# Optimization experiments

Measured on AMD Instinct MI355X. Metric: run time of the kernel, lower is better.

The kernel has to match this reference:

```python
import jax, jax.numpy as jnp
import numpy as np

COSINE_SIM_SCALE = 8.0  # default scale in flash-cosine-sim-attention
LN_EPS = 1e-5
HEADS = 8

def _l2norm(t, eps=1e-12):
    return t * jax.lax.rsqrt(jnp.sum(t * t, axis=-1, keepdims=True) + eps)

def setup_inputs() -> dict:
    key = jax.random.key(0)
    k1, k2, k3 = jax.random.split(key, 3)
    b, n, dim = 2, 2048, 1024
    inner = 512  # heads * dim_head
    return {
        "x": jax.random.normal(k1, (b, n, dim), dtype=jnp.float32),
        "ln_w": jnp.ones((dim,), dtype=jnp.float32),
        "ln_b": jnp.zeros((dim,), dtype=jnp.float32),
        "w_qkv": jax.random.normal(k2, (dim, 3 * inner), dtype=jnp.float32) * 0.02,
        "w_out": jax.random.normal(k3, (inner, dim), dtype=jnp.float32) * 0.02,
    }

def reference(x, ln_w, ln_b, w_qkv, w_out):
    b, n, dim = x.shape
    h = HEADS
    # LayerNorm
    mu = jnp.mean(x, axis=-1, keepdims=True)
    var = jnp.mean(jnp.square(x - mu), axis=-1, keepdims=True)
    xn = (x - mu) * jax.lax.rsqrt(var + LN_EPS) * ln_w + ln_b
    # QKV projection, split into heads: b n (h d) -> b h n d
    qkv = xn @ w_qkv
    q, k, v = jnp.split(qkv, 3, axis=-1)
    def to_heads(t):
        return t.reshape(b, n, h, -1).transpose(0, 2, 1, 3)
    q, k, v = map(to_heads, (q, k, v))
    # cosine-sim attention: l2-normalize q, k then scaled dot product
    q = _l2norm(q)
    k = _l2norm(k)
    sim = jnp.einsum('bhid,bhjd->bhij', q, k) * COSINE_SIM_SCALE
    causal_mask = jnp.tril(jnp.ones((n, n), dtype=bool))
    sim = jnp.where(causal_mask, sim, jnp.finfo(sim.dtype).min)
    attn = jax.nn.softmax(sim, axis=-1)
    o = jnp.einsum('bhij,bhjd->bhid', attn, v)
    # b h n d -> b n (h d)
    o = o.transpose(0, 2, 1, 3).reshape(b, n, -1)
    return o @ w_out
```

## Files before the change

### kernel.cpp

```cpp
#include <hip/hip_runtime.h>
#include <hip/hip_bf16.h>

typedef __attribute__((ext_vector_type(8))) __bf16 bf16x8;
typedef __attribute__((ext_vector_type(4))) __bf16 bf16x4;
typedef __attribute__((ext_vector_type(4))) float f32x4;

#define B_     2
#define N_     2048
#define DIM_   1024
#define INNER_ 512
#define H_     8
#define DH_    64
#define ROWS_  (B_ * N_)
#define QKVN_  (3 * INNER_)
#define SEGROWS_ 5120

static __device__ __forceinline__ f32x4 mfma16(bf16x8 a, bf16x8 b, f32x4 c) {
    return __builtin_amdgcn_mfma_f32_16x16x32_bf16(a, b, c, 0, 0, 0);
}

static __device__ __forceinline__ void gld_lds16(const void* g, void* l) {
    __builtin_amdgcn_global_load_lds((const __attribute__((address_space(1))) void*)g,
                                     (__attribute__((address_space(3))) void*)l, 16, 0, 0);
}

__global__ __launch_bounds__(256) void ln_kernel(const float* __restrict__ x,
                                                 const float* __restrict__ w,
                                                 const float* __restrict__ bb,
                                                 __bf16* __restrict__ xn) {
    int row = blockIdx.x;
    int tid = threadIdx.x;
    const float* xr = x + (size_t)row * DIM_;
    f32x4 xv = *reinterpret_cast<const f32x4*>(xr + tid * 4);
    float s  = xv.x + xv.y + xv.z + xv.w;
    float sq = xv.x * xv.x + xv.y * xv.y + xv.z * xv.z + xv.w * xv.w;
#pragma unroll
    for (int m = 1; m < 64; m <<= 1) {
        s  += __shfl_xor(s, m);
        sq += __shfl_xor(sq, m);
    }
    __shared__ float red[2][4];
    int wid = tid >> 6, lane = tid & 63;
    if (lane == 0) { red[0][wid] = s; red[1][wid] = sq; }
    __syncthreads();
    s  = red[0][0] + red[0][1] + red[0][2] + red[0][3];
    sq = red[1][0] + red[1][1] + red[1][2] + red[1][3];
    float mu   = s * (1.0f / DIM_);
    float var  = sq * (1.0f / DIM_) - mu * mu;
    float rstd = rsqrtf(var + 1e-5f);
    f32x4 wv = *reinterpret_cast<const f32x4*>(w  + tid * 4);
    f32x4 bv = *reinterpret_cast<const f32x4*>(bb + tid * 4);
    bf16x4 o;
#pragma unroll
    for (int j = 0; j < 4; ++j) o[j] = (__bf16)((xv[j] - mu) * rstd * wv[j] + bv[j]);
    *reinterpret_cast<bf16x4*>(xn + (size_t)row * DIM_ + tid * 4) = o;
}

__global__ __launch_bounds__(256) void transpose_cast(const float* __restrict__ in,
                                                      __bf16* __restrict__ out,
                                                      int K, int N) {
    __shared__ float t[64][65];
    int n0 = blockIdx.x * 64, k0 = blockIdx.y * 64;
    int w = threadIdx.x >> 6, lane = threadIdx.x & 63;
#pragma unroll
    for (int i = 0; i < 16; ++i) {
        int k = 16 * w + i;
        t[k][lane] = in[(size_t)(k0 + k) * N + n0 + lane];
    }
    __syncthreads();
#pragma unroll
    for (int i = 0; i < 16; ++i) {
        int n = 16 * w + i;
        out[(size_t)(n0 + n) * K + k0 + lane] = (__bf16)t[lane][n];
    }
}

__global__ __launch_bounds__(256) void gemm_qkv(const __bf16* __restrict__ A,
                                                const __bf16* __restrict__ Bt,
                                                __bf16* __restrict__ Qh,
                                                __bf16* __restrict__ Kh,
                                                __bf16* __restrict__ Vrow) {
    const int K = DIM_;
    __shared__ __bf16 As[128 * 32];
    __shared__ __bf16 Bs[128 * 32];
    int tid = threadIdx.x;
    int w = tid >> 6, lane = tid & 63;
    int lr = lane & 15, lg = lane >> 4;
    int m0 = blockIdx.y * 128, n0 = blockIdx.x * 128;
    int wm = (w >> 1) * 64, wn = (w & 1) * 64;
    int srow = tid >> 2, sc = tid & 3;
    const __bf16* Ab = A  + (size_t)m0 * K;
    const __bf16* Bb = Bt + (size_t)n0 * K;
    f32x4 acc[4][4];
#pragma unroll
    for (int mi = 0; mi < 4; ++mi)
#pragma unroll
        for (int ci = 0; ci < 4; ++ci) acc[mi][ci] = f32x4{0.f, 0.f, 0.f, 0.f};
    for (int k0 = 0; k0 < K; k0 += 32) {
        __syncthreads();
#pragma unroll
        for (int q = 0; q < 2; ++q) {
            int row = q * 64 + srow;
            int cs = sc ^ (row & 3);
            gld_lds16(Ab + (size_t)row * K + k0 + 8 * cs, &As[(size_t)row * 32 + sc * 8]);
            gld_lds16(Bb + (size_t)row * K + k0 + 8 * cs, &Bs[(size_t)row * 32 + sc * 8]);
        }
        __syncthreads();
        bf16x8 af[4], bfr[4];
#pragma unroll
        for (int mi = 0; mi < 4; ++mi) {
            int r = wm + 16 * mi + lr;
            af[mi] = *reinterpret_cast<const bf16x8*>(&As[r * 32 + 8 * (lg ^ (r & 3))]);
        }
#pragma unroll
        for (int ci = 0; ci < 4; ++ci) {
            int r = wn + 16 * ci + lr;
            bfr[ci] = *reinterpret_cast<const bf16x8*>(&Bs[r * 32 + 8 * (lg ^ (r & 3))]);
        }
#pragma unroll
        for (int mi = 0; mi < 4; ++mi)
#pragma unroll
            for (int ci = 0; ci < 4; ++ci)
                acc[mi][ci] = mfma16(af[mi], bfr[ci], acc[mi][ci]);
    }
    int u = (n0 + wn) >> 6;
    bool isV = (u >= 16);
    float smul = (u < 8) ? 8.0f : 1.0f;
    __bf16* base;
    if (u < 8)       base = Qh   + (size_t)u * N_ * DH_;
    else if (u < 16) base = Kh   + (size_t)(u - 8) * N_ * DH_;
    else             base = Vrow + (size_t)(u - 16) * N_ * DH_;
#pragma unroll
    for (int mi = 0; mi < 4; ++mi)
#pragma unroll
        for (int r = 0; r < 4; ++r) {
            int grow = m0 + wm + 16 * mi + 4 * lg + r;
            int b = grow >> 11, n = grow & 2047;
            float sc2 = 1.0f;
            if (!isV) {
                float t = 0.f;
#pragma unroll
                for (int ci = 0; ci < 4; ++ci) t += acc[mi][ci][r] * acc[mi][ci][r];
#pragma unroll
                for (int m = 1; m < 16; m <<= 1) t += __shfl_xor(t, m);
                sc2 = rsqrtf(t + 1e-12f) * smul;
            }
            __bf16* dst = base + ((size_t)b * H_ * N_ + n) * DH_;
#pragma unroll
            for (int ci = 0; ci < 4; ++ci)
                dst[16 * ci + lr] = (__bf16)(acc[mi][ci][r] * sc2);
        }
}

template <typename OutT>
__global__ __launch_bounds__(256) void gemm_bt(const __bf16* __restrict__ A,
                                               const __bf16* __restrict__ Bt,
                                               OutT* __restrict__ C,
                                               int M, int N, int K) {
    __shared__ __bf16 As[128 * 32];
    __shared__ __bf16 Bs[128 * 32];
    int tid = threadIdx.x;
    int w = tid >> 6, lane = tid & 63;
    int lr = lane & 15, lg = lane >> 4;
    int m0 = blockIdx.y * 128, n0 = blockIdx.x * 128;
    int wm = (w >> 1) * 64, wn = (w & 1) * 64;
    int srow = tid >> 2, sc = tid & 3;
    const __bf16* Ab = A  + (size_t)m0 * K;
    const __bf16* Bb = Bt + (size_t)n0 * K;
    f32x4 acc[4][4];
#pragma unroll
    for (int mi = 0; mi < 4; ++mi)
#pragma unroll
        for (int ci = 0; ci < 4; ++ci) acc[mi][ci] = f32x4{0.f, 0.f, 0.f, 0.f};
    for (int k0 = 0; k0 < K; k0 += 32) {
        __syncthreads();
#pragma unroll
        for (int q = 0; q < 2; ++q) {
            int row = q * 64 + srow;
            int cs = sc ^ (row & 3);
            gld_lds16(Ab + (size_t)row * K + k0 + 8 * cs, &As[(size_t)row * 32 + sc * 8]);
            gld_lds16(Bb + (size_t)row * K + k0 + 8 * cs, &Bs[(size_t)row * 32 + sc * 8]);
        }
        __syncthreads();
        bf16x8 af[4], bfr[4];
#pragma unroll
        for (int mi = 0; mi < 4; ++mi) {
            int r = wm + 16 * mi + lr;
            af[mi] = *reinterpret_cast<const bf16x8*>(&As[r * 32 + 8 * (lg ^ (r & 3))]);
        }
#pragma unroll
        for (int ci = 0; ci < 4; ++ci) {
            int r = wn + 16 * ci + lr;
            bfr[ci] = *reinterpret_cast<const bf16x8*>(&Bs[r * 32 + 8 * (lg ^ (r & 3))]);
        }
#pragma unroll
        for (int mi = 0; mi < 4; ++mi)
#pragma unroll
            for (int ci = 0; ci < 4; ++ci)
                acc[mi][ci] = mfma16(af[mi], bfr[ci], acc[mi][ci]);
    }
#pragma unroll
    for (int mi = 0; mi < 4; ++mi)
#pragma unroll
        for (int ci = 0; ci < 4; ++ci)
#pragma unroll
            for (int r = 0; r < 4; ++r)
                C[(size_t)(m0 + wm + 16 * mi + 4 * lg + r) * N + n0 + wn + 16 * ci + lr] =
                    (OutT)acc[mi][ci][r];
}

__global__ __launch_bounds__(256) void vtrans(const __bf16* __restrict__ Vrow,
                                              __bf16* __restrict__ Vt) {
    __shared__ __bf16 t[64][66];
    int bh = blockIdx.y, n0 = blockIdx.x * 64;
    int w = threadIdx.x >> 6, lane = threadIdx.x & 63;
#pragma unroll
    for (int i = 0; i < 16; ++i) {
        int nl = 16 * w + i;
        t[nl][lane] = Vrow[((size_t)bh * N_ + n0 + nl) * DH_ + lane];
    }
    __syncthreads();
#pragma unroll
    for (int i = 0; i < 16; ++i) {
        int d = 16 * w + i;
        Vt[(size_t)bh * DH_ * N_ + (size_t)d * N_ + n0 + lane] = t[lane][d];
    }
}

__global__ __launch_bounds__(256) void attn_kernel(const __bf16* __restrict__ Qh,
                                                   const __bf16* __restrict__ Kh,
                                                   const __bf16* __restrict__ Vt,
                                                   float* __restrict__ Opart,
                                                   float* __restrict__ ml) {
    __shared__ __bf16 Ks[2][64 * 64];
    __shared__ __bf16 Vs[2][64 * 64];
    __shared__ __bf16 pl[4][16 * 64];
    int bh = blockIdx.x;
    int idx = blockIdx.y;
    int s, qt;
    if (idx < 32)      { s = 0; qt = 31 - idx; }
    else if (idx < 56) { s = 1; qt = 31 - (idx - 32); }
    else if (idx < 72) { s = 2; qt = 31 - (idx - 56); }
    else               { s = 3; qt = 31 - (idx - 72); }
    int jt0 = 8 * s;
    int jt1 = min(8 * s + 7, qt);
    int tid = threadIdx.x;
    int w = tid >> 6, lane = tid & 63;
    int lr = lane & 15, lg = lane >> 4;
    int qb = qt * 64;
    int qrow = qb + 16 * w;
    const __bf16* Qp = Qh + (size_t)bh * N_ * DH_;
    const __bf16* Kp = Kh + (size_t)bh * N_ * DH_;
    const __bf16* Vp = Vt + (size_t)bh * DH_ * N_;
    bf16x8 qf0 = *reinterpret_cast<const bf16x8*>(Qp + (size_t)(qrow + lr) * DH_ + 8 * lg);
    bf16x8 qf1 = *reinterpret_cast<const bf16x8*>(Qp + (size_t)(qrow + lr) * DH_ + 32 + 8 * lg);
    f32x4 oacc[4];
#pragma unroll
    for (int c = 0; c < 4; ++c) oacc[c] = f32x4{0.f, 0.f, 0.f, 0.f};
    float m_r[4], l_r[4];
#pragma unroll
    for (int r = 0; r < 4; ++r) { m_r[r] = -1e30f; l_r[r] = 0.f; }
    int srow = tid >> 3, sc = tid & 7;

    auto stage = [&](int buf, int jb) {
#pragma unroll
        for (int q = 0; q < 2; ++q) {
            int row = q * 32 + srow;
            int cs = sc ^ (row & 7);
            gld_lds16(Kp + (size_t)(jb + row) * DH_ + 8 * cs,
                      &Ks[buf][(size_t)row * 64 + sc * 8]);
            gld_lds16(Vp + (size_t)row * N_ + jb + 8 * cs,
                      &Vs[buf][(size_t)row * 64 + sc * 8]);
        }
    };

    stage(0, jt0 * 64);
    __syncthreads();
    int cur = 0;
    for (int jt = jt0; jt <= jt1; ++jt) {
        int jb = jt * 64;
        if (jt < jt1) stage(cur ^ 1, jb + 64);
        const __bf16* ks = &Ks[cur][0];
        const __bf16* vs = &Vs[cur][0];
        f32x4 sm[4];
#pragma unroll
        for (int ch = 0; ch < 4; ++ch) {
            int row = 16 * ch + lr;
            bf16x8 k0 = *reinterpret_cast<const bf16x8*>(&ks[row * 64 + 8 * (lg ^ (row & 7))]);
            bf16x8 k1 = *reinterpret_cast<const bf16x8*>(&ks[row * 64 + 8 * ((4 + lg) ^ (row & 7))]);
            f32x4 t = f32x4{0.f, 0.f, 0.f, 0.f};
            t = mfma16(qf0, k0, t);
            t = mfma16(qf1, k1, t);
            sm[ch] = t;
        }
        if (jt == qt) {
#pragma unroll
            for (int ch = 0; ch < 4; ++ch)
#pragma unroll
                for (int r = 0; r < 4; ++r) {
                    int qi = qrow + 4 * lg + r;
                    int j  = jb + 16 * ch + lr;
                    if (j > qi) sm[ch][r] = -1e30f;
                }
        }
        float fs[4];
#pragma unroll
        for (int r = 0; r < 4; ++r) {
            float pm = fmaxf(fmaxf(sm[0][r], sm[1][r]), fmaxf(sm[2][r], sm[3][r]));
#pragma unroll
            for (int msk = 1; msk < 16; msk <<= 1) pm = fmaxf(pm, __shfl_xor(pm, msk));
            float mn = fmaxf(m_r[r], pm);
            fs[r] = __expf(m_r[r] - mn);
            m_r[r] = mn;
        }
        f32x4 p[4];
#pragma unroll
        for (int ch = 0; ch < 4; ++ch)
#pragma unroll
            for (int r = 0; r < 4; ++r) p[ch][r] = __expf(sm[ch][r] - m_r[r]);
#pragma unroll
        for (int r = 0; r < 4; ++r) {
            float rs = p[0][r] + p[1][r] + p[2][r] + p[3][r];
#pragma unroll
            for (int msk = 1; msk < 16; msk <<= 1) rs += __shfl_xor(rs, msk);
            l_r[r] = l_r[r] * fs[r] + rs;
        }
#pragma unroll
        for (int dc = 0; dc < 4; ++dc)
#pragma unroll
            for (int r = 0; r < 4; ++r) oacc[dc][r] *= fs[r];
        __bf16* plw = &pl[w][0];
#pragma unroll
        for (int ch = 0; ch < 4; ++ch)
#pragma unroll
            for (int r = 0; r < 4; ++r) {
                int row = 4 * lg + r, col = 16 * ch + lr;
                plw[row * 64 + (((col >> 3) ^ (row & 7)) << 3) + (col & 7)] = (__bf16)p[ch][r];
            }
        bf16x8 pf0 = *reinterpret_cast<const bf16x8*>(&plw[lr * 64 + ((lg ^ (lr & 7)) << 3)]);
        bf16x8 pf1 = *reinterpret_cast<const bf16x8*>(&plw[lr * 64 + (((4 + lg) ^ (lr & 7)) << 3)]);
#pragma unroll
        for (int dc = 0; dc < 4; ++dc) {
            int row = 16 * dc + lr;
            bf16x8 v0 = *reinterpret_cast<const bf16x8*>(&vs[row * 64 + 8 * (lg ^ (row & 7))]);
            bf16x8 v1 = *reinterpret_cast<const bf16x8*>(&vs[row * 64 + 8 * ((4 + lg) ^ (row & 7))]);
            oacc[dc] = mfma16(pf0, v0, oacc[dc]);
            oacc[dc] = mfma16(pf1, v1, oacc[dc]);
        }
        __syncthreads();
        cur ^= 1;
    }
    int soff = 2048 * s - 256 * s * (s - 1);
#pragma unroll
    for (int r = 0; r < 4; ++r) {
        int n = qrow + 4 * lg + r;
        size_t ridx = (size_t)bh * SEGROWS_ + soff + (n - 512 * s);
#pragma unroll
        for (int dc = 0; dc < 4; ++dc)
            Opart[ridx * 64 + 16 * dc + lr] = oacc[dc][r];
        if (lr == 0) {
            ml[ridx * 2]     = m_r[r];
            ml[ridx * 2 + 1] = l_r[r];
        }
    }
}

__global__ __launch_bounds__(256) void combine_kernel(const float* __restrict__ Opart,
                                                      const float* __restrict__ ml,
                                                      __bf16* __restrict__ Obp) {
    int gid = blockIdx.x * 4 + (threadIdx.x >> 6);
    int lane = threadIdx.x & 63;
    int bh = gid >> 11, n = gid & 2047;
    int smax = n >> 9;
    float mstar = -1e30f;
#pragma unroll
    for (int s = 0; s < 4; ++s)
        if (s <= smax) {
            int soff = 2048 * s - 256 * s * (s - 1);
            size_t ridx = (size_t)bh * SEGROWS_ + soff + (n - 512 * s);
            mstar = fmaxf(mstar, ml[ridx * 2]);
        }
    float acc = 0.f, lsum = 0.f;
#pragma unroll
    for (int s = 0; s < 4; ++s)
        if (s <= smax) {
            int soff = 2048 * s - 256 * s * (s - 1);
            size_t ridx = (size_t)bh * SEGROWS_ + soff + (n - 512 * s);
            float wgt = __expf(ml[ridx * 2] - mstar);
            acc  += wgt * Opart[ridx * 64 + lane];
            lsum += wgt * ml[ridx * 2 + 1];
        }
    int b = bh >> 3, h = bh & 7;
    Obp[((size_t)(b * N_ + n)) * INNER_ + h * DH_ + lane] = (__bf16)(acc / lsum);
}

extern "C" void kernel_launch(void* const* d_in, const int* in_sizes, int n_in,
                              void* d_out, int out_size, void* d_ws, size_t ws_size,
                              hipStream_t stream) {
    const float* x    = (const float*)d_in[0];
    const float* lnw  = (const float*)d_in[1];
    const float* lnb  = (const float*)d_in[2];
    const float* wqkv = (const float*)d_in[3];
    const float* wout = (const float*)d_in[4];
    float* out = (float*)d_out;

    char* ws = (char*)d_ws;
    size_t off = 0;
    auto alloc = [&](size_t bytes) -> char* {
        char* p = ws + off;
        off += (bytes + 255) & ~(size_t)255;
        return p;
    };
    __bf16* xn    = (__bf16*)alloc((size_t)ROWS_ * DIM_ * 2);
    __bf16* wqkvT = (__bf16*)alloc((size_t)QKVN_ * DIM_ * 2);
    __bf16* woutT = (__bf16*)alloc((size_t)DIM_ * INNER_ * 2);
    __bf16* Qhp   = (__bf16*)alloc((size_t)B_ * H_ * N_ * DH_ * 2);
    __bf16* Khp   = (__bf16*)alloc((size_t)B_ * H_ * N_ * DH_ * 2);
    __bf16* Vrow  = (__bf16*)alloc((size_t)B_ * H_ * N_ * DH_ * 2);
    __bf16* Vtp   = (__bf16*)alloc((size_t)B_ * H_ * DH_ * N_ * 2);
    __bf16* Obp   = (__bf16*)alloc((size_t)ROWS_ * INNER_ * 2);
    float*  Opart = (float*)alloc((size_t)B_ * H_ * SEGROWS_ * DH_ * 4);
    float*  mlb   = (float*)alloc((size_t)B_ * H_ * SEGROWS_ * 2 * 4);
    if (off > ws_size) return;

    transpose_cast<<<dim3(QKVN_ / 64, DIM_ / 64), 256, 0, stream>>>(wqkv, wqkvT, DIM_, QKVN_);
    transpose_cast<<<dim3(DIM_ / 64, INNER_ / 64), 256, 0, stream>>>(wout, woutT, INNER_, DIM_);
    ln_kernel<<<ROWS_, 256, 0, stream>>>(x, lnw, lnb, xn);
    gemm_qkv<<<dim3(QKVN_ / 128, ROWS_ / 128), 256, 0, stream>>>(xn, wqkvT, Qhp, Khp, Vrow);
    vtrans<<<dim3(N_ / 64, B_ * H_), 256, 0, stream>>>(Vrow, Vtp);
    attn_kernel<<<dim3(B_ * H_, 80), 256, 0, stream>>>(Qhp, Khp, Vtp, Opart, mlb);
    combine_kernel<<<(ROWS_ * H_) / 4, 256, 0, stream>>>(Opart, mlb, Obp);
    gemm_bt<float><<<dim3(DIM_ / 128, ROWS_ / 128), 256, 0, stream>>>(Obp, woutT, out, ROWS_, DIM_, INNER_);
}
```

Baseline: 182.9 us.

## Use fixed softmax max from cosine-sim bound and compute row sums via MFMA

Because q and k are l2-normalized, scores are bounded by the scale, so the online-softmax running max is replaced by a fixed constant. Q is prescaled by 8*log2(e) so exp2 can be used directly. Row sums come from an extra MFMA against a ones vector instead of shuffle reductions. This removes the max/sum shuffles and rescaling in the attention kernel and the max pass in the combine kernel, and the grid is flattened to 1D. In exchange it relies on the cosine bound and risks underflow for rows whose scores sit far below the maximum.

```diff
diff --git a/kernel.cpp b/kernel.cpp
--- a/kernel.cpp
+++ b/kernel.cpp
@@ -14,6 +14,8 @@
 #define ROWS_  (B_ * N_)
 #define QKVN_  (3 * INNER_)
 #define SEGROWS_ 5120
+#define QSCALE_ 11.5415603f
+#define MAXL2_  11.5415603f
 
 static __device__ __forceinline__ f32x4 mfma16(bf16x8 a, bf16x8 b, f32x4 c) {
     return __builtin_amdgcn_mfma_f32_16x16x32_bf16(a, b, c, 0, 0, 0);
@@ -125,7 +127,7 @@
     }
     int u = (n0 + wn) >> 6;
     bool isV = (u >= 16);
-    float smul = (u < 8) ? 8.0f : 1.0f;
+    float smul = (u < 8) ? QSCALE_ : 1.0f;
     __bf16* base;
     if (u < 8)       base = Qh   + (size_t)u * N_ * DH_;
     else if (u < 16) base = Kh   + (size_t)(u - 8) * N_ * DH_;
@@ -231,35 +233,35 @@
                                                    const __bf16* __restrict__ Kh,
                                                    const __bf16* __restrict__ Vt,
                                                    float* __restrict__ Opart,
-                                                   float* __restrict__ ml) {
+                                                   float* __restrict__ lpart) {
     __shared__ __bf16 Ks[2][64 * 64];
     __shared__ __bf16 Vs[2][64 * 64];
     __shared__ __bf16 pl[4][16 * 64];
-    int bh = blockIdx.x;
-    int idx = blockIdx.y;
+    int bh  = blockIdx.x & 15;
+    int sid = blockIdx.x >> 4;
     int s, qt;
-    if (idx < 32)      { s = 0; qt = 31 - idx; }
-    else if (idx < 56) { s = 1; qt = 31 - (idx - 32); }
-    else if (idx < 72) { s = 2; qt = 31 - (idx - 56); }
-    else               { s = 3; qt = 31 - (idx - 72); }
+    if (sid < 32)      { s = 0; qt = 31 - sid; }
+    else if (sid < 56) { s = 1; qt = 31 - (sid - 32); }
+    else if (sid < 72) { s = 2; qt = 31 - (sid - 56); }
+    else               { s = 3; qt = 31 - (sid - 72); }
     int jt0 = 8 * s;
     int jt1 = min(8 * s + 7, qt);
     int tid = threadIdx.x;
     int w = tid >> 6, lane = tid & 63;
     int lr = lane & 15, lg = lane >> 4;
-    int qb = qt * 64;
-    int qrow = qb + 16 * w;
+    int qrow = qt * 64 + 16 * w;
     const __bf16* Qp = Qh + (size_t)bh * N_ * DH_;
     const __bf16* Kp = Kh + (size_t)bh * N_ * DH_;
     const __bf16* Vp = Vt + (size_t)bh * DH_ * N_;
     bf16x8 qf0 = *reinterpret_cast<const bf16x8*>(Qp + (size_t)(qrow + lr) * DH_ + 8 * lg);
     bf16x8 qf1 = *reinterpret_cast<const bf16x8*>(Qp + (size_t)(qrow + lr) * DH_ + 32 + 8 * lg);
+    bf16x8 ones;
+#pragma unroll
+    for (int j = 0; j < 8; ++j) ones[j] = (__bf16)1.0f;
     f32x4 oacc[4];
+    f32x4 oacc4 = f32x4{0.f, 0.f, 0.f, 0.f};
 #pragma unroll
     for (int c = 0; c < 4; ++c) oacc[c] = f32x4{0.f, 0.f, 0.f, 0.f};
-    float m_r[4], l_r[4];
-#pragma unroll
-    for (int r = 0; r < 4; ++r) { m_r[r] = -1e30f; l_r[r] = 0.f; }
     int srow = tid >> 3, sc = tid & 7;
 
     auto stage = [&](int buf, int jb) {
@@ -293,42 +295,20 @@
             t = mfma16(qf1, k1, t);
             sm[ch] = t;
         }
-        if (jt == qt) {
-#pragma unroll
-            for (int ch = 0; ch < 4; ++ch)
-#pragma unroll
-                for (int r = 0; r < 4; ++r) {
+        f32x4 p[4];
+        bool diag = (jt == qt);
+#pragma unroll
+        for (int ch = 0; ch < 4; ++ch)
+#pragma unroll
+            for (int r = 0; r < 4; ++r) {
+                float pv = exp2f(sm[ch][r] - MAXL2_);
+                if (diag) {
                     int qi = qrow + 4 * lg + r;
                     int j  = jb + 16 * ch + lr;
-                    if (j > qi) sm[ch][r] = -1e30f;
+                    if (j > qi) pv = 0.f;
                 }
-        }
-        float fs[4];
-#pragma unroll
-        for (int r = 0; r < 4; ++r) {
-            float pm = fmaxf(fmaxf(sm[0][r], sm[1][r]), fmaxf(sm[2][r], sm[3][r]));
-#pragma unroll
-            for (int msk = 1; msk < 16; msk <<= 1) pm = fmaxf(pm, __shfl_xor(pm, msk));
-            float mn = fmaxf(m_r[r], pm);
-            fs[r] = __expf(m_r[r] - mn);
-            m_r[r] = mn;
-        }
-        f32x4 p[4];
-#pragma unroll
-        for (int ch = 0; ch < 4; ++ch)
-#pragma unroll
-            for (int r = 0; r < 4; ++r) p[ch][r] = __expf(sm[ch][r] - m_r[r]);
-#pragma unroll
-        for (int r = 0; r < 4; ++r) {
-            float rs = p[0][r] + p[1][r] + p[2][r] + p[3][r];
-#pragma unroll
-            for (int msk = 1; msk < 16; msk <<= 1) rs += __shfl_xor(rs, msk);
-            l_r[r] = l_r[r] * fs[r] + rs;
-        }
-#pragma unroll
-        for (int dc = 0; dc < 4; ++dc)
-#pragma unroll
-            for (int r = 0; r < 4; ++r) oacc[dc][r] *= fs[r];
+                p[ch][r] = pv;
+            }
         __bf16* plw = &pl[w][0];
 #pragma unroll
         for (int ch = 0; ch < 4; ++ch)
@@ -347,6 +327,8 @@
             oacc[dc] = mfma16(pf0, v0, oacc[dc]);
             oacc[dc] = mfma16(pf1, v1, oacc[dc]);
         }
+        oacc4 = mfma16(pf0, ones, oacc4);
+        oacc4 = mfma16(pf1, ones, oacc4);
         __syncthreads();
         cur ^= 1;
     }
@@ -358,37 +340,25 @@
 #pragma unroll
         for (int dc = 0; dc < 4; ++dc)
             Opart[ridx * 64 + 16 * dc + lr] = oacc[dc][r];
-        if (lr == 0) {
-            ml[ridx * 2]     = m_r[r];
-            ml[ridx * 2 + 1] = l_r[r];
-        }
+        if (lr == 0) lpart[ridx] = oacc4[r];
     }
 }
 
 __global__ __launch_bounds__(256) void combine_kernel(const float* __restrict__ Opart,
-                                                      const float* __restrict__ ml,
+                                                      const float* __restrict__ lpart,
                                                       __bf16* __restrict__ Obp) {
     int gid = blockIdx.x * 4 + (threadIdx.x >> 6);
     int lane = threadIdx.x & 63;
     int bh = gid >> 11, n = gid & 2047;
     int smax = n >> 9;
-    float mstar = -1e30f;
+    float acc = 0.f, lsum = 0.f;
 #pragma unroll
     for (int s = 0; s < 4; ++s)
         if (s <= smax) {
             int soff = 2048 * s - 256 * s * (s - 1);
             size_t ridx = (size_t)bh * SEGROWS_ + soff + (n - 512 * s);
-            mstar = fmaxf(mstar, ml[ridx * 2]);
-        }
-    float acc = 0.f, lsum = 0.f;
-#pragma unroll
-    for (int s = 0; s < 4; ++s)
-        if (s <= smax) {
-            int soff = 2048 * s - 256 * s * (s - 1);
-            size_t ridx = (size_t)bh * SEGROWS_ + soff + (n - 512 * s);
-            float wgt = __expf(ml[ridx * 2] - mstar);
-            acc  += wgt * Opart[ridx * 64 + lane];
-            lsum += wgt * ml[ridx * 2 + 1];
+            acc  += Opart[ridx * 64 + lane];
+            lsum += lpart[ridx];
         }
     int b = bh >> 3, h = bh & 7;
     Obp[((size_t)(b * N_ + n)) * INNER_ + h * DH_ + lane] = (__bf16)(acc / lsum);
@@ -420,7 +390,7 @@
     __bf16* Vtp   = (__bf16*)alloc((size_t)B_ * H_ * DH_ * N_ * 2);
     __bf16* Obp   = (__bf16*)alloc((size_t)ROWS_ * INNER_ * 2);
     float*  Opart = (float*)alloc((size_t)B_ * H_ * SEGROWS_ * DH_ * 4);
-    float*  mlb   = (float*)alloc((size_t)B_ * H_ * SEGROWS_ * 2 * 4);
+    float*  lbuf  = (float*)alloc((size_t)B_ * H_ * SEGROWS_ * 4);
     if (off > ws_size) return;
 
     transpose_cast<<<dim3(QKVN_ / 64, DIM_ / 64), 256, 0, stream>>>(wqkv, wqkvT, DIM_, QKVN_);
@@ -428,7 +398,7 @@
     ln_kernel<<<ROWS_, 256, 0, stream>>>(x, lnw, lnb, xn);
     gemm_qkv<<<dim3(QKVN_ / 128, ROWS_ / 128), 256, 0, stream>>>(xn, wqkvT, Qhp, Khp, Vrow);
     vtrans<<<dim3(N_ / 64, B_ * H_), 256, 0, stream>>>(Vrow, Vtp);
-    attn_kernel<<<dim3(B_ * H_, 80), 256, 0, stream>>>(Qhp, Khp, Vtp, Opart, mlb);
-    combine_kernel<<<(ROWS_ * H_) / 4, 256, 0, stream>>>(Opart, mlb, Obp);
+    attn_kernel<<<1280, 256, 0, stream>>>(Qhp, Khp, Vtp, Opart, lbuf);
+    combine_kernel<<<(ROWS_ * H_) / 4, 256, 0, stream>>>(Opart, lbuf, Obp);
     gemm_bt<float><<<dim3(DIM_ / 128, ROWS_ / 128), 256, 0, stream>>>(Obp, woutT, out, ROWS_, DIM_, INNER_);
 }
```

Result: faster. 168.2 us (-8.0%).
